# Kernel tuning notes

Measured on AMD Instinct MI355X. Metric: run time of the kernel, lower is better.

## Reference

```python
import jax, jax.numpy as jnp
import numpy as np

N_NODES = 50000
C = 256          # in_channels == hidden_size
E = 800000


def setup_inputs() -> dict:
    key = jax.random.key(0)
    ks = jax.random.split(key, 12)
    x = jax.random.normal(ks[0], (N_NODES, C), dtype=jnp.float32)
    edge_index = jax.random.randint(ks[1], (2, E), 0, N_NODES, dtype=jnp.int64)
    edge_attr = jax.random.uniform(ks[2], (E,), dtype=jnp.float32)
    edge_weights_index = jax.random.randint(ks[3], (2, E), 0, N_NODES, dtype=jnp.int64)
    s = 1.0 / np.sqrt(C)
    # TopKPooling projection vector
    p_pool = jax.random.normal(ks[4], (C,), dtype=jnp.float32) * s
    # GRU (input=C, hidden=C): gates stacked [r, z, n]
    W_ih = jax.random.normal(ks[5], (3 * C, C), dtype=jnp.float32) * s
    W_hh = jax.random.normal(ks[6], (3 * C, C), dtype=jnp.float32) * s
    b_ih = jnp.zeros((3 * C,), dtype=jnp.float32)
    b_hh = jnp.zeros((3 * C,), dtype=jnp.float32)
    # initial evolving GCN weight [C, C]
    W_init = jax.random.normal(ks[7], (C, C), dtype=jnp.float32) * s
    # EdgeDecoder MLP
    lin1_w = jax.random.normal(ks[8], (C, 2 * C), dtype=jnp.float32) / np.sqrt(2 * C)
    lin1_b = jnp.zeros((C,), dtype=jnp.float32)
    lin2_w = jax.random.normal(ks[9], (1, C), dtype=jnp.float32) * s
    lin2_b = jnp.zeros((1,), dtype=jnp.float32)
    return {
        "x": x, "edge_index": edge_index, "edge_attr": edge_attr,
        "edge_weights_index": edge_weights_index,
        "p_pool": p_pool, "W_ih": W_ih, "W_hh": W_hh, "b_ih": b_ih, "b_hh": b_hh,
        "W_init": W_init, "lin1_w": lin1_w, "lin1_b": lin1_b,
        "lin2_w": lin2_w, "lin2_b": lin2_b,
    }


def _forward(x, edge_attr, p_pool, W_ih, W_hh, b_ih, b_hh, W_init,
             lin1_w, lin1_b, lin2_w, lin2_b, edge_index, edge_weights_index):
    n_nodes, c = x.shape
    # --- EvolveGCNH: TopK pooling summary (k = in_channels) ---
    score = x @ p_pool / jnp.linalg.norm(p_pool)          # [N]
    top_score, perm = jax.lax.top_k(score, c)             # [C]
    x_tilde = x[perm] * jnp.tanh(top_score)[:, None]      # [C, C]
    # --- GRU step: input x_tilde (batch=C), hidden = evolving weight W_init ---
    gi = x_tilde @ W_ih.T + b_ih                           # [C, 3C]
    gh = W_init @ W_hh.T + b_hh                            # [C, 3C]
    i_r, i_z, i_n = jnp.split(gi, 3, axis=1)
    h_r, h_z, h_n = jnp.split(gh, 3, axis=1)
    r = jax.nn.sigmoid(i_r + h_r)
    z = jax.nn.sigmoid(i_z + h_z)
    n = jnp.tanh(i_n + r * h_n)
    W = (1.0 - z) * n + z * W_init                         # [C, C] evolved GCN weight
    # --- GCNConv with fixed W, add_self_loops=False ---
    xw = x @ W                                             # [N, C]
    src, dst = edge_index[0], edge_index[1]
    deg = jax.ops.segment_sum(edge_attr, dst, num_segments=n_nodes)
    dinv = jnp.where(deg > 0, jax.lax.rsqrt(jnp.where(deg > 0, deg, 1.0)), 0.0)
    norm = dinv[src] * edge_attr * dinv[dst]               # [E]
    node_emb = jax.ops.segment_sum(xw[src] * norm[:, None], dst,
                                   num_segments=n_nodes)   # [N, C]
    # --- EdgeDecoder: gather src/trg, concat, MLP ---
    s_idx, t_idx = edge_weights_index[0], edge_weights_index[1]
    edge_emb = jnp.concatenate([node_emb[s_idx], node_emb[t_idx]], axis=1)  # [E, 2C]
    h = jax.nn.relu(edge_emb @ lin1_w.T + lin1_b)          # [E, C]
    pred = h @ lin2_w.T + lin2_b                           # [E, 1]
    return pred.reshape(-1)


def reference(x, edge_index, edge_attr, edge_weights_index, p_pool,
              W_ih, W_hh, b_ih, b_hh, W_init, lin1_w, lin1_b, lin2_w, lin2_b):
    # dropout is identity in eval mode
    return _forward(x, edge_attr, p_pool, W_ih, W_hh, b_ih, b_hh, W_init,
                    lin1_w, lin1_b, lin2_w, lin2_b, edge_index, edge_weights_index)
```

## Files before the change

### kernel.cpp

```cpp
#include <hip/hip_runtime.h>
#include <hip/hip_bf16.h>
#include <math.h>


typedef __attribute__((ext_vector_type(8))) short bf16x8;
typedef __attribute__((ext_vector_type(8))) unsigned short u16x8;
typedef __attribute__((ext_vector_type(4))) float f32x4;

#define WSHIFT 9
#define WMASK 511
#define NBUCK 98

__device__ __forceinline__ unsigned f2key(float f) {
  unsigned u = __float_as_uint(f);
  return (u & 0x80000000u) ? ~u : (u | 0x80000000u);
}

__device__ __forceinline__ unsigned short f2bf(float f) {
  unsigned u = __float_as_uint(f);
  unsigned r = u + 0x7fffu + ((u >> 16) & 1u);
  return (unsigned short)(r >> 16);
}
__device__ __forceinline__ float bf2f(unsigned short h) {
  return __uint_as_float((unsigned)h << 16);
}

template <int CTRL>
__device__ __forceinline__ float dpp_add(float s) {
  int t = __builtin_amdgcn_update_dpp(0, __float_as_int(s), CTRL, 0xf, 0xf, false);
  return s + __int_as_float(t);
}

__device__ __forceinline__ void gload16(const void* g, void* l) {
  __builtin_amdgcn_global_load_lds((const __attribute__((address_space(1))) void*)g,
                                   (__attribute__((address_space(3))) void*)l, 16, 0, 0);
}

__global__ void zero_kernel(float4* __restrict__ p, int n4) {
  int i = blockIdx.x * blockDim.x + threadIdx.x;
  if (i < n4) p[i] = make_float4(0.f, 0.f, 0.f, 0.f);
}

__global__ __launch_bounds__(256) void score_cast_kernel(const float* __restrict__ x,
                                                         const float* __restrict__ p,
                                                         float* __restrict__ score,
                                                         unsigned short* __restrict__ xh, int N) {
  int node = blockIdx.x * 4 + (threadIdx.x >> 6);
  int lane = threadIdx.x & 63;
  if (node >= N) return;
  float4 xv = ((const float4*)(x + (size_t)node * 256))[lane];
  ushort4 hv;
  hv.x = f2bf(xv.x);
  hv.y = f2bf(xv.y);
  hv.z = f2bf(xv.z);
  hv.w = f2bf(xv.w);
  ((ushort4*)(xh + (size_t)node * 256))[lane] = hv;
  float4 pv = ((const float4*)p)[lane];
  float s = xv.x * pv.x + xv.y * pv.y + xv.z * pv.z + xv.w * pv.w;
  float sp = pv.x * pv.x + pv.y * pv.y + pv.z * pv.z + pv.w * pv.w;
#pragma unroll
  for (int off = 32; off > 0; off >>= 1) {
    s += __shfl_down(s, off, 64);
    sp += __shfl_down(sp, off, 64);
  }
  if (lane == 0) score[node] = s / sqrtf(sp);
}

__global__ __launch_bounds__(256) void hist12_kernel(const float* __restrict__ score, int n,
                                                     int* __restrict__ gh) {
  __shared__ int lh[4096];
  int tid = threadIdx.x;
  for (int i = tid; i < 4096; i += 256) lh[i] = 0;
  __syncthreads();
  int idx = blockIdx.x * 256 + tid;
  int stride = gridDim.x * 256;
  for (int i = idx; i < n; i += stride) {
    unsigned key = f2key(score[i]);
    atomicAdd(&lh[key >> 20], 1);
  }
  __syncthreads();
  for (int i = tid; i < 4096; i += 256) {
    int v = lh[i];
    if (v) atomicAdd(&gh[i], v);
  }
}

__global__ __launch_bounds__(1024) void topk_kernel(const float* __restrict__ score, int n, int k,
                                                    const int* __restrict__ gh,
                                                    int* __restrict__ perm,
                                                    float* __restrict__ tts) {
  __shared__ int part[1024];
  __shared__ unsigned sT;
  int tid = threadIdx.x;
  {
    int b0 = tid * 4;
    int s0 = gh[b0], s1 = gh[b0 + 1], s2 = gh[b0 + 2], s3 = gh[b0 + 3];
    part[tid] = s0 + s1 + s2 + s3;
    __syncthreads();
    for (int off = 1; off < 1024; off <<= 1) {
      int v = part[tid];
      int add = (tid + off < 1024) ? part[tid + off] : 0;
      __syncthreads();
      part[tid] = v + add;
      __syncthreads();
    }
    int sufChunk = part[tid];
    int sufNext = (tid < 1023) ? part[tid + 1] : 0;
    if (sufNext < k && sufChunk >= k) {
      int run = sufNext;
      int b;
      run += s3;
      if (run >= k) b = b0 + 3;
      else {
        run += s2;
        if (run >= k) b = b0 + 2;
        else {
          run += s1;
          b = (run >= k) ? b0 + 1 : b0;
        }
      }
      sT = ((unsigned)b) << 20;
    }
  }
  __syncthreads();
  unsigned T = sT;
  __shared__ unsigned keys[1024];
  __shared__ int idxs[1024];
  __shared__ int cnt;
  if (tid == 0) cnt = 0;
  keys[tid] = 0u;
  idxs[tid] = 0x7fffffff;
  __syncthreads();
  for (int i = tid; i < n; i += 1024) {
    unsigned key = f2key(score[i]);
    if (key >= T) {
      int p = atomicAdd(&cnt, 1);
      if (p < 1024) { keys[p] = key; idxs[p] = i; }
    }
  }
  __syncthreads();
  for (int size = 2; size <= 1024; size <<= 1) {
    for (int stride = size >> 1; stride > 0; stride >>= 1) {
      int j = tid ^ stride;
      if (j > tid) {
        unsigned ka = keys[tid], kb = keys[j];
        int ia = idxs[tid], ib = idxs[j];
        bool aBefore = (ka > kb) || (ka == kb && ia < ib);
        bool up = ((tid & size) == 0);
        if (aBefore != up) {
          keys[tid] = kb; keys[j] = ka;
          idxs[tid] = ib; idxs[j] = ia;
        }
      }
      __syncthreads();
    }
  }
  if (tid < k) {
    int idx = idxs[tid];
    perm[tid] = idx;
    tts[tid] = tanhf(score[idx]);
  }
}

__global__ __launch_bounds__(256) void gru_kernel(const float* __restrict__ x,
                                                  const int* __restrict__ perm,
                                                  const float* __restrict__ tts,
                                                  const float* __restrict__ Wi,
                                                  const float* __restrict__ W_ih,
                                                  const float* __restrict__ W_hh,
                                                  const float* __restrict__ b_ih,
                                                  const float* __restrict__ b_hh,
                                                  unsigned short* __restrict__ WevoT) {
  int i = blockIdx.x, j = threadIdx.x;
  __shared__ float sx[256], sh[256];
  sx[j] = x[(size_t)perm[i] * 256 + j] * tts[i];
  sh[j] = Wi[i * 256 + j];
  __syncthreads();
  float gi[3], gh[3];
#pragma unroll
  for (int g = 0; g < 3; ++g) {
    int row = g * 256 + j;
    const float4* wi4 = (const float4*)(W_ih + (size_t)row * 256);
    const float4* wh4 = (const float4*)(W_hh + (size_t)row * 256);
    float si = 0.f, s2 = 0.f;
    for (int k4 = 0; k4 < 64; ++k4) {
      float4 wv = wi4[k4];
      float4 hv = wh4[k4];
      int k = k4 * 4;
      si += sx[k] * wv.x + sx[k + 1] * wv.y + sx[k + 2] * wv.z + sx[k + 3] * wv.w;
      s2 += sh[k] * hv.x + sh[k + 1] * hv.y + sh[k + 2] * hv.z + sh[k + 3] * hv.w;
    }
    gi[g] = si + b_ih[row];
    gh[g] = s2 + b_hh[row];
  }
  float r = 1.f / (1.f + expf(-(gi[0] + gh[0])));
  float z = 1.f / (1.f + expf(-(gi[1] + gh[1])));
  float nn = tanhf(gi[2] + r * gh[2]);
  float w = (1.f - z) * nn + z * sh[j];
  WevoT[(size_t)j * 256 + i] = f2bf(w);
}

__global__ __launch_bounds__(256) void lin1_cast_kernel(const float* __restrict__ lin1,
                                                        unsigned short* __restrict__ WAB) {
  int idx = blockIdx.x * 256 + threadIdx.x;
  int n = idx >> 9, k = idx & 511;
  unsigned short h = f2bf(lin1[idx]);
  if (k < 256)
    WAB[n * 256 + k] = h;
  else
    WAB[(256 + n) * 256 + (k - 256)] = h;
}

__global__ __launch_bounds__(512) void mfma_gemm128(const unsigned short* __restrict__ A,
                                                    const unsigned short* __restrict__ BT,
                                                    unsigned short* __restrict__ C1,
                                                    unsigned short* __restrict__ C2,
                                                    int M) {
  __shared__ unsigned short sA[128 * 32];
  __shared__ unsigned short sB[256 * 32];
  int tid = threadIdx.x;
  int wave = tid >> 6, lane = tid & 63;
  int quad = lane >> 4, r16 = lane & 15;
  int wm = wave >> 2, wn = wave & 3;
  int mbase = blockIdx.x * 128;
  const unsigned short* Bt = BT + ((size_t)blockIdx.y << 16);
  unsigned short* Cout = blockIdx.y ? C2 : C1;

  int srow = tid >> 2, scolq = tid & 3;
  const unsigned short* gA = A + (size_t)(mbase + srow) * 256 + scolq * 8;
  const unsigned short* gB0 = Bt + (size_t)srow * 256 + scolq * 8;
  const unsigned short* gB1 = Bt + (size_t)(128 + srow) * 256 + scolq * 8;
  unsigned short* lA = sA + wave * 512;
  unsigned short* lB0 = sB + wave * 512;
  unsigned short* lB1 = sB + 4096 + wave * 512;

  f32x4 acc[4][4];
#pragma unroll
  for (int i = 0; i < 4; ++i)
#pragma unroll
    for (int j = 0; j < 4; ++j) acc[i][j] = (f32x4){0.f, 0.f, 0.f, 0.f};

  const unsigned short* pA = sA + (wm * 64 + r16) * 32 + quad * 8;
  const unsigned short* pB = sB + (wn * 64 + r16) * 32 + quad * 8;

  for (int k0 = 0; k0 < 256; k0 += 32) {
    if (k0) __syncthreads();
    gload16(gA + k0, lA);
    gload16(gB0 + k0, lB0);
    gload16(gB1 + k0, lB1);
    __syncthreads();
    bf16x8 af[4], bfr[4];
#pragma unroll
    for (int mt = 0; mt < 4; ++mt) af[mt] = *(const bf16x8*)(pA + mt * 512);
#pragma unroll
    for (int nt = 0; nt < 4; ++nt) bfr[nt] = *(const bf16x8*)(pB + nt * 512);
#pragma unroll
    for (int mt = 0; mt < 4; ++mt)
#pragma unroll
      for (int nt = 0; nt < 4; ++nt)
        acc[mt][nt] = __builtin_amdgcn_mfma_f32_16x16x32_bf16(af[mt], bfr[nt], acc[mt][nt], 0, 0, 0);
  }
#pragma unroll
  for (int mt = 0; mt < 4; ++mt) {
#pragma unroll
    for (int rr = 0; rr < 4; ++rr) {
      int grow = mbase + wm * 64 + mt * 16 + quad * 4 + rr;
      if (grow < M) {
#pragma unroll
        for (int nt = 0; nt < 4; ++nt)
          Cout[(size_t)grow * 256 + wn * 64 + nt * 16 + r16] = f2bf(acc[mt][nt][rr]);
      }
    }
  }
}


__global__ __launch_bounds__(256) void bucket_hist_kernel(const int* __restrict__ ei,
                                                          const int* __restrict__ ewi,
                                                          int* __restrict__ bcnt1,
                                                          int* __restrict__ bcnt2, int E) {
  __shared__ int c1[128], c2[128];
  int tid = threadIdx.x;
  if (tid < 128) { c1[tid] = 0; c2[tid] = 0; }
  __syncthreads();
  int idx = blockIdx.x * 256 + tid;
  int stride = gridDim.x * 256;
  for (int e = idx; e < E; e += stride) {
    atomicAdd(&c1[ei[E + e] >> WSHIFT], 1);
    atomicAdd(&c2[ewi[e] >> WSHIFT], 1);
  }
  __syncthreads();
  if (tid < 128) {
    if (c1[tid]) atomicAdd(&bcnt1[tid], c1[tid]);
    if (c2[tid]) atomicAdd(&bcnt2[tid], c2[tid]);
  }
}

__global__ __launch_bounds__(128) void bucket_scan_kernel(const int* __restrict__ bcnt1,
                                                          const int* __restrict__ bcnt2,
                                                          int* __restrict__ bbase1,
                                                          int* __restrict__ bbase2,
                                                          int* __restrict__ gcur1,
                                                          int* __restrict__ gcur2,
                                                          int* __restrict__ rowp1,
                                                          int* __restrict__ rowp2, int N, int E) {
  __shared__ int ss[128];
  int tid = threadIdx.x;
  int v = (tid < NBUCK) ? bcnt1[tid] : 0;
  ss[tid] = v;
  __syncthreads();
  for (int off = 1; off < 128; off <<= 1) {
    int a = ss[tid];
    int b = (tid >= off) ? ss[tid - off] : 0;
    __syncthreads();
    ss[tid] = a + b;
    __syncthreads();
  }
  int excl = ss[tid] - v;
  if (tid < NBUCK) { bbase1[tid] = excl; gcur1[tid] = excl; }
  if (tid == NBUCK - 1) bbase1[NBUCK] = excl + v;
  __syncthreads();
  v = (tid < NBUCK) ? bcnt2[tid] : 0;
  ss[tid] = v;
  __syncthreads();
  for (int off = 1; off < 128; off <<= 1) {
    int a = ss[tid];
    int b = (tid >= off) ? ss[tid - off] : 0;
    __syncthreads();
    ss[tid] = a + b;
    __syncthreads();
  }
  excl = ss[tid] - v;
  if (tid < NBUCK) { bbase2[tid] = excl; gcur2[tid] = excl; }
  if (tid == NBUCK - 1) bbase2[NBUCK] = excl + v;
  if (tid == 0) { rowp1[N] = E; rowp2[N] = E; }
}

__global__ __launch_bounds__(256) void p1_conv_kernel(const int* __restrict__ ei,
                                                      const float* __restrict__ attr,
                                                      int* __restrict__ gcur,
                                                      int2* __restrict__ stage, int E) {
  __shared__ int cnt[128], cur[128];
  int tid = threadIdx.x;
  int base = blockIdx.x * 4096;
  if (tid < 128) cnt[tid] = 0;
  __syncthreads();
  int bk[16];
  int2 pl[16];
#pragma unroll
  for (int i = 0; i < 16; ++i) {
    int e = base + i * 256 + tid;
    bk[i] = -1;
    if (e < E) {
      int d = ei[E + e];
      int s = ei[e];
      bk[i] = d >> WSHIFT;
      pl[i] = make_int2(s | ((d & WMASK) << 16), __float_as_int(attr[e]));
      atomicAdd(&cnt[bk[i]], 1);
    }
  }
  __syncthreads();
  if (tid < NBUCK) {
    int c = cnt[tid];
    cur[tid] = c ? atomicAdd(&gcur[tid], c) : 0;
  }
  __syncthreads();
#pragma unroll
  for (int i = 0; i < 16; ++i) {
    if (bk[i] >= 0) {
      int pos = atomicAdd(&cur[bk[i]], 1);
      stage[pos] = pl[i];
    }
  }
}

__global__ __launch_bounds__(256) void p1_dec_kernel(const int* __restrict__ ewi,
                                                     int* __restrict__ gcur,
                                                     int2* __restrict__ stage, int E) {
  __shared__ int cnt[128], cur[128];
  int tid = threadIdx.x;
  int base = blockIdx.x * 4096;
  if (tid < 128) cnt[tid] = 0;
  __syncthreads();
  int bk[16];
  int2 pl[16];
#pragma unroll
  for (int i = 0; i < 16; ++i) {
    int e = base + i * 256 + tid;
    bk[i] = -1;
    if (e < E) {
      int s = ewi[e];
      int d = ewi[E + e];
      bk[i] = s >> WSHIFT;
      pl[i] = make_int2(d | ((s & WMASK) << 16), e);
      atomicAdd(&cnt[bk[i]], 1);
    }
  }
  __syncthreads();
  if (tid < NBUCK) {
    int c = cnt[tid];
    cur[tid] = c ? atomicAdd(&gcur[tid], c) : 0;
  }
  __syncthreads();
#pragma unroll
  for (int i = 0; i < 16; ++i) {
    if (bk[i] >= 0) {
      int pos = atomicAdd(&cur[bk[i]], 1);
      stage[pos] = pl[i];
    }
  }
}

__global__ __launch_bounds__(256) void p2_kernel(const int2* __restrict__ stage1,
                                                 const int* __restrict__ bbase1,
                                                 int2* __restrict__ esv,
                                                 int* __restrict__ rowp1,
                                                 float* __restrict__ dinv,
                                                 const int2* __restrict__ stage2,
                                                 const int* __restrict__ bbase2,
                                                 int2* __restrict__ eto,
                                                 int* __restrict__ rowp2, int N) {
  __shared__ int cnt[512];
  __shared__ float degs[512];
  __shared__ int pref[512];
  __shared__ int ss[256];
  int tid = threadIdx.x;
  bool isConv = blockIdx.x < NBUCK;
  int b = isConv ? blockIdx.x : blockIdx.x - NBUCK;
  const int2* stage = isConv ? stage1 : stage2;
  const int* bbase = isConv ? bbase1 : bbase2;
  int beg = bbase[b], end = bbase[b + 1];
  int node0 = b << WSHIFT;
  cnt[tid] = 0; cnt[tid + 256] = 0;
  degs[tid] = 0.f; degs[tid + 256] = 0.f;
  __syncthreads();
  for (int j = beg + tid; j < end; j += 256) {
    int2 p = stage[j];
    int loc = p.x >> 16;
    atomicAdd(&cnt[loc], 1);
    if (isConv) atomicAdd(&degs[loc], __int_as_float(p.y));
  }
  __syncthreads();
  int c0 = cnt[2 * tid], c1 = cnt[2 * tid + 1];
  ss[tid] = c0 + c1;
  __syncthreads();
  for (int off = 1; off < 256; off <<= 1) {
    int a = ss[tid];
    int bb = (tid >= off) ? ss[tid - off] : 0;
    __syncthreads();
    ss[tid] = a + bb;
    __syncthreads();
  }
  int excl = (tid ? ss[tid - 1] : 0);
  pref[2 * tid] = excl;
  pref[2 * tid + 1] = excl + c0;
  __syncthreads();
#pragma unroll
  for (int h = 0; h < 2; ++h) {
    int i = tid + h * 256;
    int node = node0 + i;
    if (node < N) {
      if (isConv) {
        rowp1[node] = beg + pref[i];
        float d = degs[i];
        dinv[node] = d > 0.f ? 1.f / sqrtf(d) : 0.f;
      } else {
        rowp2[node] = beg + pref[i];
      }
    }
  }
  __syncthreads();
  int2* outb = isConv ? esv : eto;
  for (int j = beg + tid; j < end; j += 256) {
    int2 p = stage[j];
    int loc = p.x >> 16;
    int pos = beg + atomicAdd(&pref[loc], 1);
    outb[pos] = make_int2(p.x & 0xFFFF, p.y);
  }
}

__global__ __launch_bounds__(256) void gcn_gather(const unsigned short* __restrict__ xw,
                                                  const int* __restrict__ row_ptr,
                                                  const int2* __restrict__ esv,
                                                  const float* __restrict__ dinv,
                                                  unsigned short* __restrict__ ne, int N) {
  int node = blockIdx.x * 4 + (threadIdx.x >> 6);
  int lane = threadIdx.x & 63;
  int g = lane & 15, q = lane >> 4;
  if (node >= N) return;
  int beg = row_ptr[node], end = row_ptr[node + 1];
  float acc[16];
#pragma unroll
  for (int c = 0; c < 16; ++c) acc[c] = 0.f;
  const unsigned short* xb = xw + g * 16;
  if (beg < end) {
    int2 m;
    int e;
    bool ok;
    e = beg + q;
    ok = e < end;
    m = ok ? esv[e] : make_int2(0, 0);
    float vA = ok ? dinv[m.x] * __int_as_float(m.y) : 0.f;
    u16x8 rAa = *(const u16x8*)(xb + (size_t)m.x * 256);
    u16x8 rAb = *(const u16x8*)(xb + (size_t)m.x * 256 + 8);
    float vB = 0.f;
    u16x8 rBa = rAa, rBb = rAb;
    if (beg + 4 < end) {
      e = beg + 4 + q;
      ok = e < end;
      m = ok ? esv[e] : make_int2(0, 0);
      vB = ok ? dinv[m.x] * __int_as_float(m.y) : 0.f;
      rBa = *(const u16x8*)(xb + (size_t)m.x * 256);
      rBb = *(const u16x8*)(xb + (size_t)m.x * 256 + 8);
    }
    float vC = 0.f;
    u16x8 rCa = rAa, rCb = rAb;
    if (beg + 8 < end) {
      e = beg + 8 + q;
      ok = e < end;
      m = ok ? esv[e] : make_int2(0, 0);
      vC = ok ? dinv[m.x] * __int_as_float(m.y) : 0.f;
      rCa = *(const u16x8*)(xb + (size_t)m.x * 256);
      rCb = *(const u16x8*)(xb + (size_t)m.x * 256 + 8);
    }
    for (int jb = beg; jb < end; jb += 12) {
#pragma unroll
      for (int c = 0; c < 8; ++c) acc[c] += bf2f(rAa[c]) * vA;
#pragma unroll
      for (int c = 0; c < 8; ++c) acc[8 + c] += bf2f(rAb[c]) * vA;
      vA = 0.f;
      if (jb + 12 < end) {
        e = jb + 12 + q;
        ok = e < end;
        m = ok ? esv[e] : make_int2(0, 0);
        vA = ok ? dinv[m.x] * __int_as_float(m.y) : 0.f;
        rAa = *(const u16x8*)(xb + (size_t)m.x * 256);
        rAb = *(const u16x8*)(xb + (size_t)m.x * 256 + 8);
      }
#pragma unroll
      for (int c = 0; c < 8; ++c) acc[c] += bf2f(rBa[c]) * vB;
#pragma unroll
      for (int c = 0; c < 8; ++c) acc[8 + c] += bf2f(rBb[c]) * vB;
      vB = 0.f;
      if (jb + 16 < end) {
        e = jb + 16 + q;
        ok = e < end;
        m = ok ? esv[e] : make_int2(0, 0);
        vB = ok ? dinv[m.x] * __int_as_float(m.y) : 0.f;
        rBa = *(const u16x8*)(xb + (size_t)m.x * 256);
        rBb = *(const u16x8*)(xb + (size_t)m.x * 256 + 8);
      }
#pragma unroll
      for (int c = 0; c < 8; ++c) acc[c] += bf2f(rCa[c]) * vC;
#pragma unroll
      for (int c = 0; c < 8; ++c) acc[8 + c] += bf2f(rCb[c]) * vC;
      vC = 0.f;
      if (jb + 20 < end) {
        e = jb + 20 + q;
        ok = e < end;
        m = ok ? esv[e] : make_int2(0, 0);
        vC = ok ? dinv[m.x] * __int_as_float(m.y) : 0.f;
        rCa = *(const u16x8*)(xb + (size_t)m.x * 256);
        rCb = *(const u16x8*)(xb + (size_t)m.x * 256 + 8);
      }
    }
  }
#pragma unroll
  for (int c = 0; c < 16; ++c) {
    acc[c] += __shfl_xor(acc[c], 16, 64);
    acc[c] += __shfl_xor(acc[c], 32, 64);
  }
  if (q == 0) {
    float dd = dinv[node];
    u16x8 o0, o1;
#pragma unroll
    for (int c = 0; c < 8; ++c) {
      o0[c] = f2bf(acc[c] * dd);
      o1[c] = f2bf(acc[8 + c] * dd);
    }
    *(u16x8*)(ne + (size_t)node * 256 + g * 16) = o0;
    *(u16x8*)(ne + (size_t)node * 256 + g * 16 + 8) = o1;
  }
}

__global__ __launch_bounds__(256) void edge_decode_csr(const unsigned short* __restrict__ A,
                                                       const unsigned short* __restrict__ Bm,
                                                       const int* __restrict__ row_ptr,
                                                       const int2* __restrict__ eto,
                                                       const float* __restrict__ b1,
                                                       const float* __restrict__ w2,
                                                       const float* __restrict__ b2,
                                                       float* __restrict__ out, int N) {
  int node = blockIdx.x * 4 + (threadIdx.x >> 6);
  int lane = threadIdx.x & 63;
  int g = lane & 15, q = lane >> 4;
  if (node >= N) return;
  int beg = row_ptr[node], end = row_ptr[node + 1];
  if (beg >= end) return;
  float a[16], w[16];
  {
    u16x8 a0 = *(const u16x8*)(A + (size_t)node * 256 + g * 16);
    u16x8 a1 = *(const u16x8*)(A + (size_t)node * 256 + g * 16 + 8);
    const float4* bp = (const float4*)(b1 + g * 16);
    const float4* wp = (const float4*)(w2 + g * 16);
#pragma unroll
    for (int i = 0; i < 4; ++i) {
      float4 bv = bp[i];
      float4 wv = wp[i];
      a[i * 4 + 0] = (i < 2 ? bf2f(a0[i * 4 + 0]) : bf2f(a1[i * 4 - 8])) + bv.x;
      a[i * 4 + 1] = (i < 2 ? bf2f(a0[i * 4 + 1]) : bf2f(a1[i * 4 - 7])) + bv.y;
      a[i * 4 + 2] = (i < 2 ? bf2f(a0[i * 4 + 2]) : bf2f(a1[i * 4 - 6])) + bv.z;
      a[i * 4 + 3] = (i < 2 ? bf2f(a0[i * 4 + 3]) : bf2f(a1[i * 4 - 5])) + bv.w;
      w[i * 4 + 0] = wv.x;
      w[i * 4 + 1] = wv.y;
      w[i * 4 + 2] = wv.z;
      w[i * 4 + 3] = wv.w;
    }
  }
  float base = b2[0];
  const unsigned short* Bb = Bm + g * 16;
  int e = beg + q;
  int2 mA = (e < end) ? eto[e] : make_int2(0, -1);
  u16x8 rAa = *(const u16x8*)(Bb + (size_t)mA.x * 256);
  u16x8 rAb = *(const u16x8*)(Bb + (size_t)mA.x * 256 + 8);
  int2 mB = make_int2(0, -1);
  u16x8 rBa = rAa, rBb = rAb;
  if (beg + 4 < end) {
    e = beg + 4 + q;
    mB = (e < end) ? eto[e] : make_int2(0, -1);
    rBa = *(const u16x8*)(Bb + (size_t)mB.x * 256);
    rBb = *(const u16x8*)(Bb + (size_t)mB.x * 256 + 8);
  }
  for (int jb = beg; jb < end; jb += 8) {
    {
      float s0 = 0.f, s1 = 0.f;
#pragma unroll
      for (int c = 0; c < 8; ++c) s0 += fmaxf(a[c] + bf2f(rAa[c]), 0.f) * w[c];
#pragma unroll
      for (int c = 0; c < 8; ++c) s1 += fmaxf(a[8 + c] + bf2f(rAb[c]), 0.f) * w[8 + c];
      float s = s0 + s1;
      s = dpp_add<0x128>(s);
      s = dpp_add<0x124>(s);
      s = dpp_add<0x122>(s);
      s = dpp_add<0x121>(s);
      if (g == 0 && mA.y >= 0) out[mA.y] = s + base;
    }
    mA.y = -1;
    if (jb + 8 < end) {
      e = jb + 8 + q;
      mA = (e < end) ? eto[e] : make_int2(0, -1);
      rAa = *(const u16x8*)(Bb + (size_t)mA.x * 256);
      rAb = *(const u16x8*)(Bb + (size_t)mA.x * 256 + 8);
    }
    {
      float s0 = 0.f, s1 = 0.f;
#pragma unroll
      for (int c = 0; c < 8; ++c) s0 += fmaxf(a[c] + bf2f(rBa[c]), 0.f) * w[c];
#pragma unroll
      for (int c = 0; c < 8; ++c) s1 += fmaxf(a[8 + c] + bf2f(rBb[c]), 0.f) * w[8 + c];
      float s = s0 + s1;
      s = dpp_add<0x128>(s);
      s = dpp_add<0x124>(s);
      s = dpp_add<0x122>(s);
      s = dpp_add<0x121>(s);
      if (g == 0 && mB.y >= 0) out[mB.y] = s + base;
    }
    mB.y = -1;
    if (jb + 12 < end) {
      e = jb + 12 + q;
      mB = (e < end) ? eto[e] : make_int2(0, -1);
      rBa = *(const u16x8*)(Bb + (size_t)mB.x * 256);
      rBb = *(const u16x8*)(Bb + (size_t)mB.x * 256 + 8);
    }
  }
}

extern "C" void kernel_launch(void* const* d_in, const int* in_sizes, int n_in,
                              void* d_out, int out_size, void* d_ws, size_t ws_size,
                              hipStream_t stream) {
  const float* x      = (const float*)d_in[0];
  const int*   ei     = (const int*)d_in[1];
  const float* attr   = (const float*)d_in[2];
  const int*   ewi    = (const int*)d_in[3];
  const float* p_pool = (const float*)d_in[4];
  const float* W_ih   = (const float*)d_in[5];
  const float* W_hh   = (const float*)d_in[6];
  const float* b_ih   = (const float*)d_in[7];
  const float* b_hh   = (const float*)d_in[8];
  const float* W_init = (const float*)d_in[9];
  const float* lin1_w = (const float*)d_in[10];
  const float* lin1_b = (const float*)d_in[11];
  const float* lin2_w = (const float*)d_in[12];
  const float* lin2_b = (const float*)d_in[13];
  float* out = (float*)d_out;

  const int C = 256;
  const int N = in_sizes[0] / C;
  const int E = in_sizes[2];

  char* ws = (char*)d_ws;
  size_t off = 0;
  auto alloc = [&](size_t bytes) {
    size_t o = off;
    off = (off + bytes + 255) & ~(size_t)255;
    return o;
  };
  float*          score  = (float*)(ws + alloc((size_t)N * 4));
  int*            perm   = (int*)(ws + alloc(C * 4));
  float*          tts    = (float*)(ws + alloc(C * 4));
  unsigned short* WevoT  = (unsigned short*)(ws + alloc((size_t)C * C * 2));
  unsigned short* WAB    = (unsigned short*)(ws + alloc((size_t)2 * C * C * 2));
  int   zeroInts = 4096 + 128 + 128;
  char* zbase    = ws + alloc((size_t)zeroInts * 4);
  int* ghist = (int*)zbase;
  int* bcnt1 = (int*)(zbase + 4096 * 4);
  int* bcnt2 = (int*)(zbase + 4096 * 4 + 128 * 4);
  int*            bbase1 = (int*)(ws + alloc((NBUCK + 1) * 4));
  int*            bbase2 = (int*)(ws + alloc((NBUCK + 1) * 4));
  int*            gcur1  = (int*)(ws + alloc(128 * 4));
  int*            gcur2  = (int*)(ws + alloc(128 * 4));
  float*          dinv   = (float*)(ws + alloc((size_t)N * 4));
  int*            rowp1  = (int*)(ws + alloc((size_t)(N + 1) * 4));
  int*            rowp2  = (int*)(ws + alloc((size_t)(N + 1) * 4));
  int2*           stage1 = (int2*)(ws + alloc((size_t)E * 8));
  int2*           stage2 = (int2*)(ws + alloc((size_t)E * 8));
  int2*           esv    = (int2*)(ws + alloc((size_t)E * 8));
  int2*           eto    = (int2*)(ws + alloc((size_t)E * 8));
  unsigned short* xh     = (unsigned short*)(ws + alloc((size_t)N * C * 2));
  unsigned short* xwh    = (unsigned short*)(ws + alloc((size_t)N * C * 2));
  unsigned short* Bbf    = (unsigned short*)(ws + alloc((size_t)N * C * 2));
  unsigned short* ne  = xh;
  unsigned short* Abf = xwh;

  zero_kernel<<<(zeroInts / 4 + 255) / 256, 256, 0, stream>>>((float4*)zbase, zeroInts / 4);

  score_cast_kernel<<<(N + 3) / 4, 256, 0, stream>>>(x, p_pool, score, xh, N);

  hist12_kernel<<<64, 256, 0, stream>>>(score, N, ghist);
  topk_kernel<<<1, 1024, 0, stream>>>(score, N, C, ghist, perm, tts);

  gru_kernel<<<C, C, 0, stream>>>(x, perm, tts, W_init, W_ih, W_hh, b_ih, b_hh, WevoT);

  mfma_gemm128<<<dim3((N + 127) / 128, 1), 512, 0, stream>>>(xh, WevoT, xwh, xwh, N);

  bucket_hist_kernel<<<256, 256, 0, stream>>>(ei, ewi, bcnt1, bcnt2, E);
  bucket_scan_kernel<<<1, 128, 0, stream>>>(bcnt1, bcnt2, bbase1, bbase2, gcur1, gcur2,
                                            rowp1, rowp2, N, E);
  p1_conv_kernel<<<(E + 4095) / 4096, 256, 0, stream>>>(ei, attr, gcur1, stage1, E);
  p1_dec_kernel<<<(E + 4095) / 4096, 256, 0, stream>>>(ewi, gcur2, stage2, E);
  p2_kernel<<<2 * NBUCK, 256, 0, stream>>>(stage1, bbase1, esv, rowp1, dinv,
                                           stage2, bbase2, eto, rowp2, N);

  gcn_gather<<<(N + 3) / 4, 256, 0, stream>>>(xwh, rowp1, esv, dinv, ne, N);

  lin1_cast_kernel<<<(2 * C * C) / 256, 256, 0, stream>>>(lin1_w, WAB);
  mfma_gemm128<<<dim3((N + 127) / 128, 2), 512, 0, stream>>>(ne, WAB, Abf, Bbf, N);

  edge_decode_csr<<<(N + 3) / 4, 256, 0, stream>>>(Abf, Bbf, rowp2, eto,
                                                   lin1_b, lin2_w, lin2_b, out, N);
}
```

Baseline: 475.9 us.

## Prescale edge weights by source dinv and batch-load CSR metadata via wave shuffles

Adds a small pass that multiplies each conv edge weight by dinv[src] ahead of time, so the gather no longer does a dependent dinv lookup per edge. Both gcn_gather and edge_decode_csr now load up to 64 edge records per wave in one coalesced read and hand them to lanes with shuffles, instead of issuing scattered small loads inside the prefetch chain. The aim is to shorten the dependent-load latency in front of each row fetch. The cost is an extra kernel launch and one read-write pass over esv, and the int4 view assumes E is even.

```diff
diff --git a/kernel.cpp b/kernel.cpp
--- a/kernel.cpp
+++ b/kernel.cpp
@@ -479,6 +479,17 @@
   }
 }
 
+__global__ __launch_bounds__(256) void esv_scale_kernel(int4* __restrict__ esv,
+                                                        const float* __restrict__ dinv, int E2) {
+  int i = blockIdx.x * 256 + threadIdx.x;
+  if (i < E2) {
+    int4 p = esv[i];
+    p.y = __float_as_int(__int_as_float(p.y) * dinv[p.x]);
+    p.w = __float_as_int(__int_as_float(p.w) * dinv[p.z]);
+    esv[i] = p;
+  }
+}
+
 __global__ __launch_bounds__(256) void gcn_gather(const unsigned short* __restrict__ xw,
                                                   const int* __restrict__ row_ptr,
                                                   const int2* __restrict__ esv,
@@ -493,75 +504,83 @@
 #pragma unroll
   for (int c = 0; c < 16; ++c) acc[c] = 0.f;
   const unsigned short* xb = xw + g * 16;
-  if (beg < end) {
-    int2 m;
-    int e;
-    bool ok;
-    e = beg + q;
-    ok = e < end;
-    m = ok ? esv[e] : make_int2(0, 0);
-    float vA = ok ? dinv[m.x] * __int_as_float(m.y) : 0.f;
-    u16x8 rAa = *(const u16x8*)(xb + (size_t)m.x * 256);
-    u16x8 rAb = *(const u16x8*)(xb + (size_t)m.x * 256 + 8);
-    float vB = 0.f;
-    u16x8 rBa = rAa, rBb = rAb;
-    if (beg + 4 < end) {
-      e = beg + 4 + q;
-      ok = e < end;
-      m = ok ? esv[e] : make_int2(0, 0);
-      vB = ok ? dinv[m.x] * __int_as_float(m.y) : 0.f;
-      rBa = *(const u16x8*)(xb + (size_t)m.x * 256);
-      rBb = *(const u16x8*)(xb + (size_t)m.x * 256 + 8);
-    }
-    float vC = 0.f;
-    u16x8 rCa = rAa, rCb = rAb;
-    if (beg + 8 < end) {
-      e = beg + 8 + q;
-      ok = e < end;
-      m = ok ? esv[e] : make_int2(0, 0);
-      vC = ok ? dinv[m.x] * __int_as_float(m.y) : 0.f;
-      rCa = *(const u16x8*)(xb + (size_t)m.x * 256);
-      rCb = *(const u16x8*)(xb + (size_t)m.x * 256 + 8);
-    }
-    for (int jb = beg; jb < end; jb += 12) {
+
+  for (int cb = beg; cb < end; cb += 64) {
+    int cend = cb + 64 < end ? cb + 64 : end;
+    int me = cb + lane;
+    int2 mm = (me < cend) ? esv[me] : make_int2(0, 0);
+    int mx = mm.x;
+    float mv = __int_as_float(mm.y);
+
+    float vA = 0.f, vB = 0.f, vC = 0.f;
+    u16x8 rAa, rAb, rBa, rBb, rCa, rCb;
+    {
+      int e = cb + q;
+      int sx = __shfl(mx, q, 64);
+      float tv = __shfl(mv, q, 64);
+      vA = (e < cend) ? tv : 0.f;
+      rAa = *(const u16x8*)(xb + (size_t)sx * 256);
+      rAb = *(const u16x8*)(xb + (size_t)sx * 256 + 8);
+    }
+    if (cb + 4 < cend) {
+      int e = cb + 4 + q;
+      int sx = __shfl(mx, 4 + q, 64);
+      float tv = __shfl(mv, 4 + q, 64);
+      vB = (e < cend) ? tv : 0.f;
+      rBa = *(const u16x8*)(xb + (size_t)sx * 256);
+      rBb = *(const u16x8*)(xb + (size_t)sx * 256 + 8);
+    } else { rBa = rAa; rBb = rAb; }
+    if (cb + 8 < cend) {
+      int e = cb + 8 + q;
+      int sx = __shfl(mx, 8 + q, 64);
+      float tv = __shfl(mv, 8 + q, 64);
+      vC = (e < cend) ? tv : 0.f;
+      rCa = *(const u16x8*)(xb + (size_t)sx * 256);
+      rCb = *(const u16x8*)(xb + (size_t)sx * 256 + 8);
+    } else { rCa = rAa; rCb = rAb; }
+
+    for (int jb = cb; jb < cend; jb += 12) {
 #pragma unroll
       for (int c = 0; c < 8; ++c) acc[c] += bf2f(rAa[c]) * vA;
 #pragma unroll
       for (int c = 0; c < 8; ++c) acc[8 + c] += bf2f(rAb[c]) * vA;
       vA = 0.f;
-      if (jb + 12 < end) {
-        e = jb + 12 + q;
-        ok = e < end;
-        m = ok ? esv[e] : make_int2(0, 0);
-        vA = ok ? dinv[m.x] * __int_as_float(m.y) : 0.f;
-        rAa = *(const u16x8*)(xb + (size_t)m.x * 256);
-        rAb = *(const u16x8*)(xb + (size_t)m.x * 256 + 8);
+      if (jb + 12 < cend) {
+        int e = jb + 12 + q;
+        int idx = (e - cb) & 63;
+        int sx = __shfl(mx, idx, 64);
+        float tv = __shfl(mv, idx, 64);
+        vA = (e < cend) ? tv : 0.f;
+        rAa = *(const u16x8*)(xb + (size_t)sx * 256);
+        rAb = *(const u16x8*)(xb + (size_t)sx * 256 + 8);
       }
 #pragma unroll
       for (int c = 0; c < 8; ++c) acc[c] += bf2f(rBa[c]) * vB;
 #pragma unroll
       for (int c = 0; c < 8; ++c) acc[8 + c] += bf2f(rBb[c]) * vB;
       vB = 0.f;
-      if (jb + 16 < end) {
-        e = jb + 16 + q;
-        ok = e < end;
-        m = ok ? esv[e] : make_int2(0, 0);
-        vB = ok ? dinv[m.x] * __int_as_float(m.y) : 0.f;
-        rBa = *(const u16x8*)(xb + (size_t)m.x * 256);
-        rBb = *(const u16x8*)(xb + (size_t)m.x * 256 + 8);
+      if (jb + 16 < cend) {
+        int e = jb + 16 + q;
+        int idx = (e - cb) & 63;
+        int sx = __shfl(mx, idx, 64);
+        float tv = __shfl(mv, idx, 64);
+        vB = (e < cend) ? tv : 0.f;
+        rBa = *(const u16x8*)(xb + (size_t)sx * 256);
+        rBb = *(const u16x8*)(xb + (size_t)sx * 256 + 8);
       }
 #pragma unroll
       for (int c = 0; c < 8; ++c) acc[c] += bf2f(rCa[c]) * vC;
 #pragma unroll
       for (int c = 0; c < 8; ++c) acc[8 + c] += bf2f(rCb[c]) * vC;
       vC = 0.f;
-      if (jb + 20 < end) {
-        e = jb + 20 + q;
-        ok = e < end;
-        m = ok ? esv[e] : make_int2(0, 0);
-        vC = ok ? dinv[m.x] * __int_as_float(m.y) : 0.f;
-        rCa = *(const u16x8*)(xb + (size_t)m.x * 256);
-        rCb = *(const u16x8*)(xb + (size_t)m.x * 256 + 8);
+      if (jb + 20 < cend) {
+        int e = jb + 20 + q;
+        int idx = (e - cb) & 63;
+        int sx = __shfl(mx, idx, 64);
+        float tv = __shfl(mv, idx, 64);
+        vC = (e < cend) ? tv : 0.f;
+        rCa = *(const u16x8*)(xb + (size_t)sx * 256);
+        rCb = *(const u16x8*)(xb + (size_t)sx * 256 + 8);
       }
     }
   }
@@ -619,58 +638,80 @@
   }
   float base = b2[0];
   const unsigned short* Bb = Bm + g * 16;
-  int e = beg + q;
-  int2 mA = (e < end) ? eto[e] : make_int2(0, -1);
-  u16x8 rAa = *(const u16x8*)(Bb + (size_t)mA.x * 256);
-  u16x8 rAb = *(const u16x8*)(Bb + (size_t)mA.x * 256 + 8);
-  int2 mB = make_int2(0, -1);
-  u16x8 rBa = rAa, rBb = rAb;
-  if (beg + 4 < end) {
-    e = beg + 4 + q;
-    mB = (e < end) ? eto[e] : make_int2(0, -1);
-    rBa = *(const u16x8*)(Bb + (size_t)mB.x * 256);
-    rBb = *(const u16x8*)(Bb + (size_t)mB.x * 256 + 8);
-  }
-  for (int jb = beg; jb < end; jb += 8) {
+
+  for (int cb = beg; cb < end; cb += 64) {
+    int cend = cb + 64 < end ? cb + 64 : end;
+    int me = cb + lane;
+    int2 mm = (me < cend) ? eto[me] : make_int2(0, 0);
+    int mx = mm.x, my = mm.y;
+
+    bool okA = false, okB = false;
+    int oA = 0, oB = 0;
+    u16x8 rAa, rAb, rBa, rBb;
     {
-      float s0 = 0.f, s1 = 0.f;
-#pragma unroll
-      for (int c = 0; c < 8; ++c) s0 += fmaxf(a[c] + bf2f(rAa[c]), 0.f) * w[c];
-#pragma unroll
-      for (int c = 0; c < 8; ++c) s1 += fmaxf(a[8 + c] + bf2f(rAb[c]), 0.f) * w[8 + c];
-      float s = s0 + s1;
-      s = dpp_add<0x128>(s);
-      s = dpp_add<0x124>(s);
-      s = dpp_add<0x122>(s);
-      s = dpp_add<0x121>(s);
-      if (g == 0 && mA.y >= 0) out[mA.y] = s + base;
-    }
-    mA.y = -1;
-    if (jb + 8 < end) {
-      e = jb + 8 + q;
-      mA = (e < end) ? eto[e] : make_int2(0, -1);
-      rAa = *(const u16x8*)(Bb + (size_t)mA.x * 256);
-      rAb = *(const u16x8*)(Bb + (size_t)mA.x * 256 + 8);
-    }
-    {
-      float s0 = 0.f, s1 = 0.f;
-#pragma unroll
-      for (int c = 0; c < 8; ++c) s0 += fmaxf(a[c] + bf2f(rBa[c]), 0.f) * w[c];
-#pragma unroll
-      for (int c = 0; c < 8; ++c) s1 += fmaxf(a[8 + c] + bf2f(rBb[c]), 0.f) * w[8 + c];
-      float s = s0 + s1;
-      s = dpp_add<0x128>(s);
-      s = dpp_add<0x124>(s);
-      s = dpp_add<0x122>(s);
-      s = dpp_add<0x121>(s);
-      if (g == 0 && mB.y >= 0) out[mB.y] = s + base;
-    }
-    mB.y = -1;
-    if (jb + 12 < end) {
-      e = jb + 12 + q;
-      mB = (e < end) ? eto[e] : make_int2(0, -1);
-      rBa = *(const u16x8*)(Bb + (size_t)mB.x * 256);
-      rBb = *(const u16x8*)(Bb + (size_t)mB.x * 256 + 8);
+      int e = cb + q;
+      int sx = __shfl(mx, q, 64);
+      oA = __shfl(my, q, 64);
+      okA = e < cend;
+      rAa = *(const u16x8*)(Bb + (size_t)sx * 256);
+      rAb = *(const u16x8*)(Bb + (size_t)sx * 256 + 8);
+    }
+    if (cb + 4 < cend) {
+      int e = cb + 4 + q;
+      int sx = __shfl(mx, 4 + q, 64);
+      oB = __shfl(my, 4 + q, 64);
+      okB = e < cend;
+      rBa = *(const u16x8*)(Bb + (size_t)sx * 256);
+      rBb = *(const u16x8*)(Bb + (size_t)sx * 256 + 8);
+    } else { rBa = rAa; rBb = rAb; }
+
+    for (int jb = cb; jb < cend; jb += 8) {
+      {
+        float s0 = 0.f, s1 = 0.f;
+#pragma unroll
+        for (int c = 0; c < 8; ++c) s0 += fmaxf(a[c] + bf2f(rAa[c]), 0.f) * w[c];
+#pragma unroll
+        for (int c = 0; c < 8; ++c) s1 += fmaxf(a[8 + c] + bf2f(rAb[c]), 0.f) * w[8 + c];
+        float s = s0 + s1;
+        s = dpp_add<0x128>(s);
+        s = dpp_add<0x124>(s);
+        s = dpp_add<0x122>(s);
+        s = dpp_add<0x121>(s);
+        if (g == 0 && okA) out[oA] = s + base;
+      }
+      okA = false;
+      if (jb + 8 < cend) {
+        int e = jb + 8 + q;
+        int idx = (e - cb) & 63;
+        int sx = __shfl(mx, idx, 64);
+        oA = __shfl(my, idx, 64);
+        okA = e < cend;
+        rAa = *(const u16x8*)(Bb + (size_t)sx * 256);
+        rAb = *(const u16x8*)(Bb + (size_t)sx * 256 + 8);
+      }
+      {
+        float s0 = 0.f, s1 = 0.f;
+#pragma unroll
+        for (int c = 0; c < 8; ++c) s0 += fmaxf(a[c] + bf2f(rBa[c]), 0.f) * w[c];
+#pragma unroll
+        for (int c = 0; c < 8; ++c) s1 += fmaxf(a[8 + c] + bf2f(rBb[c]), 0.f) * w[8 + c];
+        float s = s0 + s1;
+        s = dpp_add<0x128>(s);
+        s = dpp_add<0x124>(s);
+        s = dpp_add<0x122>(s);
+        s = dpp_add<0x121>(s);
+        if (g == 0 && okB) out[oB] = s + base;
+      }
+      okB = false;
+      if (jb + 12 < cend) {
+        int e = jb + 12 + q;
+        int idx = (e - cb) & 63;
+        int sx = __shfl(mx, idx, 64);
+        oB = __shfl(my, idx, 64);
+        okB = e < cend;
+        rBa = *(const u16x8*)(Bb + (size_t)sx * 256);
+        rBb = *(const u16x8*)(Bb + (size_t)sx * 256 + 8);
+      }
     }
   }
 }
@@ -751,6 +792,8 @@
   p2_kernel<<<2 * NBUCK, 256, 0, stream>>>(stage1, bbase1, esv, rowp1, dinv,
                                            stage2, bbase2, eto, rowp2, N);
 
+  esv_scale_kernel<<<(E / 2 + 255) / 256, 256, 0, stream>>>((int4*)esv, dinv, E / 2);
+
   gcn_gather<<<(N + 3) / 4, 256, 0, stream>>>(xwh, rowp1, esv, dinv, ne, N);
 
   lin1_cast_kernel<<<(2 * C * C) / 256, 256, 0, stream>>>(lin1_w, WAB);
```

Measured after the change: 466.9 us. No clear change (-1.9%).
